# Optimization experiments

Hardware: AMD Instinct MI355X
Metric: run time of the kernel (lower is better)

The kernel has to match this reference:

```python
import jax, jax.numpy as jnp
import numpy as np
from jax import lax

B, C, T, S = 32, 122, 500, 13
WID, EMB, PROJ = 80, 8, 1024
HID = 768  # (H=1)*(W=96)*(E=8) after CNN
EPS = 1e-5
DN = ('NCHW', 'OIHW', 'NCHW')


def setup_inputs() -> dict:
    key = jax.random.key(0)
    ks = jax.random.split(key, 24)
    f32 = jnp.float32
    def n(k, shape, scale):
        return (jax.random.normal(k, shape, dtype=f32) * scale).astype(f32)
    return {
        'x': jax.random.normal(ks[0], (B, C, T), dtype=f32),
        'subject_ids': jax.random.randint(ks[1], (B,), 0, S, dtype=jnp.int32),
        'W_sub': n(ks[2], (S, T, T), 0.04),      # nn.Linear(500,500) weight per subject
        'b_sub': n(ks[3], (S, T), 0.02),
        'conv1_w': n(ks[4], (WID, 1, 1, 5), 0.3),
        'conv1_b': n(ks[5], (WID,), 0.02),
        'bn1_g': 1.0 + n(ks[6], (WID,), 0.1),
        'bn1_b': n(ks[7], (WID,), 0.1),
        'bn1_m': n(ks[8], (WID,), 0.1),
        'bn1_v': 0.5 + jax.random.uniform(ks[9], (WID,), dtype=f32),
        'conv2_w': n(ks[10], (WID, WID, C, 1), 0.01),
        'conv2_b': n(ks[11], (WID,), 0.02),
        'bn2_g': 1.0 + n(ks[12], (WID,), 0.1),
        'bn2_b': n(ks[13], (WID,), 0.1),
        'bn2_m': n(ks[14], (WID,), 0.1),
        'bn2_v': 0.5 + jax.random.uniform(ks[15], (WID,), dtype=f32),
        'proj_w': n(ks[16], (EMB, WID, 1, 1), 0.1),
        'proj_b': n(ks[17], (EMB,), 0.02),
        'mlp1_w': n(ks[18], (PROJ, HID), 0.03),
        'mlp1_b': n(ks[19], (PROJ,), 0.02),
        'mlp2_w': n(ks[20], (PROJ, PROJ), 0.03),
        'mlp2_b': n(ks[21], (PROJ,), 0.02),
        'ln_g': 1.0 + n(ks[22], (PROJ,), 0.05),
        'ln_b': n(ks[23], (PROJ,), 0.05),
    }


def _bn(h, g, b, m, v):
    # eval-mode BatchNorm2d over channel axis 1
    scale = (g / jnp.sqrt(v + EPS))[None, :, None, None]
    shift = (b - m * g / jnp.sqrt(v + EPS))[None, :, None, None]
    return h * scale + shift


def _forward(x, subject_ids, W_sub, b_sub, conv1_w, conv1_b, bn1_g, bn1_b, bn1_m, bn1_v,
             conv2_w, conv2_b, bn2_g, bn2_b, bn2_m, bn2_v, proj_w, proj_b,
             mlp1_w, mlp1_b, mlp2_w, mlp2_b, ln_g, ln_b):
    # --- per-subject routing: gather each sample's Linear(500,500) and apply ---
    Wg = W_sub[subject_ids]                       # [B,T,T] (out,in)
    bg = b_sub[subject_ids]                       # [B,T]
    out = jnp.einsum('bcs,bts->bct', x, Wg) + bg[:, None, :]
    # --- spatio-temporal CNN (eval mode: dropout = identity) ---
    h = out[:, None, :, :]                        # [B,1,C,T]
    h = lax.conv_general_dilated(h, conv1_w, (1, 1), 'VALID', dimension_numbers=DN)
    h = h + conv1_b[None, :, None, None]          # [B,80,122,496]
    h = lax.reduce_window(h, 0.0, lax.add, (1, 1, 1, 17), (1, 1, 1, 5), 'VALID') / 17.0  # [B,80,122,96]
    h = jax.nn.elu(_bn(h, bn1_g, bn1_b, bn1_m, bn1_v))
    h = lax.conv_general_dilated(h, conv2_w, (1, 1), 'VALID', dimension_numbers=DN)
    h = h + conv2_b[None, :, None, None]          # [B,80,1,96]
    h = jax.nn.elu(_bn(h, bn2_g, bn2_b, bn2_m, bn2_v))
    h = lax.conv_general_dilated(h, proj_w, (1, 1), 'VALID', dimension_numbers=DN)
    h = h + proj_b[None, :, None, None]           # [B,8,1,96]
    z = jnp.transpose(h, (0, 2, 3, 1)).reshape(h.shape[0], -1)  # [B,768]
    # --- MLP projector: Linear -> Residual(GELU+Linear) -> LayerNorm ---
    z1 = z @ mlp1_w.T + mlp1_b                    # [B,1024]
    r = jax.nn.gelu(z1, approximate=False) @ mlp2_w.T + mlp2_b
    y = z1 + r
    mu = jnp.mean(y, axis=-1, keepdims=True)
    var = jnp.var(y, axis=-1, keepdims=True)
    return (y - mu) / jnp.sqrt(var + EPS) * ln_g + ln_b


def reference(x, subject_ids, W_sub, b_sub, conv1_w, conv1_b, bn1_g, bn1_b, bn1_m, bn1_v,
              conv2_w, conv2_b, bn2_g, bn2_b, bn2_m, bn2_v, proj_w, proj_b,
              mlp1_w, mlp1_b, mlp2_w, mlp2_b, ln_g, ln_b):
    return _forward(x, subject_ids, W_sub, b_sub, conv1_w, conv1_b, bn1_g, bn1_b, bn1_m, bn1_v,
                    conv2_w, conv2_b, bn2_g, bn2_b, bn2_m, bn2_v, proj_w, proj_b,
                    mlp1_w, mlp1_b, mlp2_w, mlp2_b, ln_g, ln_b)
```

## Files before the change

### kernel.cpp

```cpp
#include <hip/hip_runtime.h>
#include <math.h>

#define BB 32
#define CC 122
#define TT 500
#define SS 13
#define WID 80
#define EMB 8
#define PROJ 1024
#define HID 768
#define TP 96
#define EPSF 1e-5f
#define KP 9760
#define KBN 305
#define KSPLIT 16

typedef float f32x4 __attribute__((ext_vector_type(4)));
typedef __bf16 bf16x8 __attribute__((ext_vector_type(8)));
typedef unsigned short u16x8 __attribute__((ext_vector_type(8)));
union BF8 { u16x8 u; bf16x8 b; };

__device__ __forceinline__ unsigned short f2bf(float f) {
    union { float f; unsigned u; } v; v.f = f;
    unsigned r = v.u + 0x7FFFu + ((v.u >> 16) & 1u);
    return (unsigned short)(r >> 16);
}

__device__ __forceinline__ float eluf(float x) {
    return x > 0.f ? x : __expf(x) - 1.f;
}

#define OFF_E    ((size_t)0)
#define OFF_XB   ((size_t)1952000)
#define OFF_WB   ((size_t)3000576)
#define OFF_W2P  ((size_t)4704512)
#define OFF_P    ((size_t)5094912)
#define OFF_PART ((size_t)20086272)
#define OFF_Z    ((size_t)24018432)
#define OFF_Z1   ((size_t)24030720)
#define OFF_G    ((size_t)24063488)
#define OFF_Y    ((size_t)24079872)
#define OFF_W1B  ((size_t)24112640)
#define OFF_W2B  ((size_t)24505856)
#define OFF_WCB  ((size_t)25030144)
#define OFF_B1F  ((size_t)25031424)
#define OFF_SC2  ((size_t)25031504)
#define OFF_SH2  ((size_t)25031584)

#define NPK_X  (2097152)
#define NPK_W  (3407872)
#define NPK_W2 (780800)
#define NPK_M1 (786432)
#define NPK_M2 (1048576)
#define NPK_TOT (NPK_X + NPK_W + NPK_W2 + NPK_M1 + NPK_M2)

__global__ __launch_bounds__(256) void k_pack(const float* __restrict__ x,
                                              const float* __restrict__ W_sub,
                                              const float* __restrict__ conv2_w,
                                              const float* __restrict__ mlp1_w,
                                              const float* __restrict__ mlp2_w,
                                              const float* __restrict__ conv1_w, const float* __restrict__ conv1_b,
                                              const float* __restrict__ g1, const float* __restrict__ b1,
                                              const float* __restrict__ m1, const float* __restrict__ v1,
                                              const float* __restrict__ conv2_b, const float* __restrict__ g2,
                                              const float* __restrict__ b2, const float* __restrict__ m2,
                                              const float* __restrict__ v2,
                                              unsigned short* __restrict__ xb,
                                              unsigned short* __restrict__ wb,
                                              unsigned short* __restrict__ w2p,
                                              unsigned short* __restrict__ w1b,
                                              unsigned short* __restrict__ w2b,
                                              unsigned short* __restrict__ wcb, float* __restrict__ bias1f,
                                              float* __restrict__ scale2, float* __restrict__ shift2f) {
    if (blockIdx.x == 0) {
        int o = threadIdx.x;
        if (o < WID) {
            float s1 = g1[o] * rsqrtf(v1[o] + EPSF);
            float sh1 = b1[o] - m1[o] * s1;
            #pragma unroll
            for (int d = 0; d < 21; d++) {
                int klo = d - 16; if (klo < 0) klo = 0;
                int khi = d;      if (khi > 4) khi = 4;
                float acc = 0.f;
                for (int k = klo; k <= khi; k++) acc += conv1_w[o*5 + k];
                wcb[o*32 + d] = f2bf(acc * s1 * (1.f/17.f));
            }
            #pragma unroll
            for (int d = 21; d < 32; d++) wcb[o*32 + d] = 0;
            bias1f[o] = conv1_b[o] * s1 + sh1;
            float s2 = g2[o] * rsqrtf(v2[o] + EPSF);
            scale2[o] = s2;
            shift2f[o] = conv2_b[o] * s2 + (b2[o] - m2[o] * s2);
        }
    }
    size_t idx = (size_t)blockIdx.x * 256 + threadIdx.x;
    if (idx >= (size_t)NPK_TOT) return;
    if (idx < NPK_X) {
        int s = idx & 511, c = (idx >> 9) & 127, b = idx >> 16;
        float v = (c < CC && s < TT) ? x[((size_t)b * CC + c) * TT + s] : 0.f;
        xb[idx] = f2bf(v);
    } else if (idx < NPK_X + NPK_W) {
        size_t j = idx - NPK_X;
        int s = j & 511, t = (j >> 9) & 511, sub = j >> 18;
        float v = (t < TT && s < TT) ? W_sub[((size_t)sub * TT + t) * TT + s] : 0.f;
        wb[j] = f2bf(v);
    } else if (idx < NPK_X + NPK_W + NPK_W2) {
        size_t j = idx - NPK_X - NPK_W;
        int o = (int)(j / KP);
        int k = (int)(j % KP);
        int c = k / WID, op = k % WID;
        w2p[j] = f2bf(conv2_w[((size_t)(o * WID + op)) * CC + c]);
    } else if (idx < NPK_X + NPK_W + NPK_W2 + NPK_M1) {
        size_t j = idx - NPK_X - NPK_W - NPK_W2;
        w1b[j] = f2bf(mlp1_w[j]);
    } else {
        size_t j = idx - NPK_X - NPK_W - NPK_W2 - NPK_M1;
        w2b[j] = f2bf(mlp2_w[j]);
    }
}

__global__ __launch_bounds__(256) void k_einsum(const unsigned short* __restrict__ xb,
                                                const unsigned short* __restrict__ wb,
                                                const int* __restrict__ sid,
                                                const float* __restrict__ b_sub,
                                                float* __restrict__ oute) {
    int t0 = blockIdx.x * 64, b = blockIdx.y;
    int s = sid[b];
    int tid = threadIdx.x, w = tid >> 6, lr = tid & 15, lg = (tid >> 4) & 3;
    const unsigned short* A0 = xb + ((size_t)(b * 128 + w * 32 + lr)) * 512 + 8 * lg;
    const unsigned short* Bb = wb + (size_t)s * 262144 + 8 * lg;
    f32x4 acc[2][4] = {};
    for (int kb = 0; kb < 512; kb += 32) {
        BF8 a0, a1;
        a0.u = *(const u16x8*)(A0 + kb);
        a1.u = *(const u16x8*)(A0 + 16 * 512 + kb);
        #pragma unroll
        for (int nt = 0; nt < 4; nt++) {
            BF8 bf; bf.u = *(const u16x8*)(Bb + (size_t)(t0 + nt * 16 + lr) * 512 + kb);
            acc[0][nt] = __builtin_amdgcn_mfma_f32_16x16x32_bf16(a0.b, bf.b, acc[0][nt], 0, 0, 0);
            acc[1][nt] = __builtin_amdgcn_mfma_f32_16x16x32_bf16(a1.b, bf.b, acc[1][nt], 0, 0, 0);
        }
    }
    const float* bg = b_sub + (size_t)s * TT;
    #pragma unroll
    for (int nt = 0; nt < 4; nt++) {
        int t = t0 + nt * 16 + lr;
        if (t < TT) {
            float bias = bg[t];
            #pragma unroll
            for (int mt = 0; mt < 2; mt++) {
                int crow = w * 32 + mt * 16 + 4 * lg;
                #pragma unroll
                for (int r = 0; r < 4; r++) {
                    int c = crow + r;
                    if (c < CC) oute[((size_t)b * CC + c) * TT + t] = acc[mt][nt][r] + bias;
                }
            }
        }
    }
}

__global__ __launch_bounds__(256) void k_fir2(const float* __restrict__ oute,
                                              const unsigned short* __restrict__ wcb,
                                              const float* __restrict__ b1f,
                                              unsigned short* __restrict__ p) {
    __shared__ float e2[2][512];
    int cp = blockIdx.x, b = blockIdx.y;
    int tid = threadIdx.x;
    int w = tid >> 6, lr = tid & 15, lg = (tid >> 4) & 3;
    if (tid < 250) {
        int cc = tid / 125, i = tid % 125;
        ((float4*)e2[cc])[i] = ((const float4*)(oute + ((size_t)b * CC + cp * 2 + cc) * TT))[i];
    }
    if (tid >= 232) {
        int j = tid - 232; int cc = j / 12, i = 500 + (j % 12);
        e2[cc][i] = 0.f;
    }
    BF8 af[5]; float4 bf4[5];
    #pragma unroll
    for (int ot = 0; ot < 5; ot++) {
        af[ot].u = *(const u16x8*)(wcb + (ot * 16 + lr) * 32 + 8 * lg);
        bf4[ot] = *(const float4*)(b1f + ot * 16 + 4 * lg);
    }
    __syncthreads();
    #pragma unroll
    for (int ui = 0; ui < 3; ui++) {
        int u = w + 4 * ui;
        int cc = u / 6, tt = u % 6;
        int t = tt * 16 + lr;
        const float* ew = e2[cc] + 5 * t + 8 * lg;
        BF8 bfr;
        #pragma unroll
        for (int j = 0; j < 8; j++) bfr.u[j] = f2bf(ew[j]);
        f32x4 acc[5] = {};
        #pragma unroll
        for (int ot = 0; ot < 5; ot++)
            acc[ot] = __builtin_amdgcn_mfma_f32_16x16x32_bf16(af[ot].b, bfr.b, acc[ot], 0, 0, 0);
        int c = cp * 2 + cc;
        unsigned short* pr = p + ((size_t)b * TP + t) * KP + (size_t)c * WID + 4 * lg;
        #pragma unroll
        for (int ot = 0; ot < 5; ot++) {
            union { unsigned short s[4]; uint2 v; } pk;
            #pragma unroll
            for (int r = 0; r < 4; r++) pk.s[r] = f2bf(eluf(acc[ot][r] + bf4[ot][r]));
            *(uint2*)(pr + ot * 16) = pk.v;
        }
    }
}

__global__ __launch_bounds__(384) void k_conv2(const unsigned short* __restrict__ p,
                                               const unsigned short* __restrict__ w2p,
                                               float* __restrict__ part) {
    int chunk = blockIdx.x, b = blockIdx.y;
    int tid = threadIdx.x, w = tid >> 6, l = tid & 63, lr = l & 15, lg = l >> 4;
    int kb0 = (chunk * KBN) / KSPLIT;
    int kb1 = ((chunk + 1) * KBN) / KSPLIT;
    const unsigned short* Brow = p + ((size_t)(b * TP + w * 16 + lr)) * KP + 8 * lg;
    const unsigned short* Arow = w2p + (size_t)lr * KP + 8 * lg;
    f32x4 acc[5] = {};
    for (int kb = kb0; kb < kb1; kb++) {
        int ko = kb * 32;
        BF8 bf; bf.u = *(const u16x8*)(Brow + ko);
        #pragma unroll
        for (int mt = 0; mt < 5; mt++) {
            BF8 af; af.u = *(const u16x8*)(Arow + (size_t)mt * 16 * KP + ko);
            acc[mt] = __builtin_amdgcn_mfma_f32_16x16x32_bf16(af.b, bf.b, acc[mt], 0, 0, 0);
        }
    }
    float* pp = part + ((size_t)(chunk * BB + b) * WID) * TP;
    int t = w * 16 + lr;
    #pragma unroll
    for (int mt = 0; mt < 5; mt++) {
        int ob = mt * 16 + 4 * lg;
        #pragma unroll
        for (int r = 0; r < 4; r++)
            pp[(size_t)(ob + r) * TP + t] = acc[mt][r];
    }
}

__global__ __launch_bounds__(256) void k_redproj(const float* __restrict__ part,
                                                 const float* __restrict__ scale2,
                                                 const float* __restrict__ shift2f,
                                                 const float* __restrict__ pw,
                                                 const float* __restrict__ pb,
                                                 unsigned short* __restrict__ zbf) {
    __shared__ float ly[WID * TP];
    __shared__ float lw[EMB * WID];
    int b = blockIdx.x, tid = threadIdx.x;
    for (int i = tid; i < EMB * WID; i += 256) lw[i] = pw[i];
    for (int i = tid; i < WID * TP; i += 256) {
        float acc = 0.f;
        #pragma unroll
        for (int ks = 0; ks < KSPLIT; ks++)
            acc += part[(size_t)(ks * BB + b) * (WID * TP) + i];
        int o = i / TP;
        ly[i] = eluf(acc * scale2[o] + shift2f[o]);
    }
    __syncthreads();
    #pragma unroll
    for (int rep = 0; rep < 3; rep++) {
        int j = tid + 256 * rep;
        int e = j & 7, t = j >> 3;
        float acc = pb[e];
        #pragma unroll 10
        for (int o = 0; o < WID; o++) acc = fmaf(ly[o * TP + t], lw[e * WID + o], acc);
        zbf[(size_t)b * HID + j] = f2bf(acc);
    }
}

__global__ __launch_bounds__(256) void k_mlp1(const unsigned short* __restrict__ zbf,
                                              const unsigned short* __restrict__ w1b,
                                              const float* __restrict__ bias,
                                              float* __restrict__ z1,
                                              unsigned short* __restrict__ gbf) {
    __shared__ float accb[2][64][4];
    int tid = threadIdx.x, w = tid >> 6, l = tid & 63, lr = l & 15, lg = l >> 4;
    int mt = w & 1, kh = w >> 1;
    int pcol = blockIdx.x * 16 + lr;
    const unsigned short* wr = w1b + (size_t)pcol * HID + kh * 384 + 8 * lg;
    const unsigned short* za = zbf + (size_t)(mt * 16 + lr) * HID + kh * 384 + 8 * lg;
    f32x4 acc = {};
    for (int kb = 0; kb < 384; kb += 32) {
        BF8 bf; bf.u = *(const u16x8*)(wr + kb);
        BF8 a;  a.u  = *(const u16x8*)(za + kb);
        acc = __builtin_amdgcn_mfma_f32_16x16x32_bf16(a.b, bf.b, acc, 0, 0, 0);
    }
    if (kh == 1) {
        #pragma unroll
        for (int r = 0; r < 4; r++) accb[mt][l][r] = acc[r];
    }
    __syncthreads();
    if (kh == 0) {
        float bs = bias[pcol];
        #pragma unroll
        for (int r = 0; r < 4; r++) {
            int row = mt * 16 + 4 * lg + r;
            float v = acc[r] + accb[mt][l][r] + bs;
            z1[(size_t)row * PROJ + pcol] = v;
            gbf[(size_t)row * PROJ + pcol] = f2bf(0.5f * v * (1.f + erff(v * 0.70710678118654752f)));
        }
    }
}

__global__ __launch_bounds__(256) void k_mlp2(const unsigned short* __restrict__ gbf,
                                              const float* __restrict__ z1,
                                              const unsigned short* __restrict__ w2b,
                                              const float* __restrict__ bias,
                                              float* __restrict__ y) {
    __shared__ float accb[2][64][4];
    int tid = threadIdx.x, w = tid >> 6, l = tid & 63, lr = l & 15, lg = l >> 4;
    int mt = w & 1, kh = w >> 1;
    int q = blockIdx.x * 16 + lr;
    const unsigned short* wr = w2b + (size_t)q * PROJ + kh * 512 + 8 * lg;
    const unsigned short* ga = gbf + (size_t)(mt * 16 + lr) * PROJ + kh * 512 + 8 * lg;
    f32x4 acc = {};
    for (int kb = 0; kb < 512; kb += 32) {
        BF8 bf; bf.u = *(const u16x8*)(wr + kb);
        BF8 a;  a.u  = *(const u16x8*)(ga + kb);
        acc = __builtin_amdgcn_mfma_f32_16x16x32_bf16(a.b, bf.b, acc, 0, 0, 0);
    }
    if (kh == 1) {
        #pragma unroll
        for (int r = 0; r < 4; r++) accb[mt][l][r] = acc[r];
    }
    __syncthreads();
    if (kh == 0) {
        float bs = bias[q];
        #pragma unroll
        for (int r = 0; r < 4; r++) {
            int row = mt * 16 + 4 * lg + r;
            y[(size_t)row * PROJ + q] = acc[r] + accb[mt][l][r] + bs + z1[(size_t)row * PROJ + q];
        }
    }
}

__global__ __launch_bounds__(256) void k_ln(const float* __restrict__ y,
                                            const float* __restrict__ lg,
                                            const float* __restrict__ lb,
                                            float* __restrict__ out) {
    int b = blockIdx.x, tid = threadIdx.x;
    const float4* yr = (const float4*)(y + (size_t)b * PROJ);
    float4 v = yr[tid];
    float s  = v.x + v.y + v.z + v.w;
    float sq = v.x*v.x + v.y*v.y + v.z*v.z + v.w*v.w;
    #pragma unroll
    for (int off = 32; off > 0; off >>= 1) {
        s  += __shfl_down(s, off);
        sq += __shfl_down(sq, off);
    }
    __shared__ float ss[4], ssq[4];
    int wv = tid >> 6, lane = tid & 63;
    if (lane == 0) { ss[wv] = s; ssq[wv] = sq; }
    __syncthreads();
    __shared__ float smu, sinv;
    if (tid == 0) {
        float Sm = ss[0] + ss[1] + ss[2] + ss[3];
        float Sq = ssq[0] + ssq[1] + ssq[2] + ssq[3];
        float mu = Sm * (1.f / PROJ);
        float var = Sq * (1.f / PROJ) - mu * mu;
        smu = mu;
        sinv = rsqrtf(var + EPSF);
    }
    __syncthreads();
    float mu = smu, inv = sinv;
    float4 g4 = ((const float4*)lg)[tid];
    float4 b4 = ((const float4*)lb)[tid];
    float4 o4;
    o4.x = (v.x - mu) * inv * g4.x + b4.x;
    o4.y = (v.y - mu) * inv * g4.y + b4.y;
    o4.z = (v.z - mu) * inv * g4.z + b4.z;
    o4.w = (v.w - mu) * inv * g4.w + b4.w;
    ((float4*)(out + (size_t)b * PROJ))[tid] = o4;
}

extern "C" void kernel_launch(void* const* d_in, const int* in_sizes, int n_in,
                              void* d_out, int out_size, void* d_ws, size_t ws_size,
                              hipStream_t stream) {
    const float* x        = (const float*)d_in[0];
    const int*   sid      = (const int*)  d_in[1];
    const float* W_sub    = (const float*)d_in[2];
    const float* b_sub    = (const float*)d_in[3];
    const float* conv1_w  = (const float*)d_in[4];
    const float* conv1_b  = (const float*)d_in[5];
    const float* bn1_g    = (const float*)d_in[6];
    const float* bn1_b    = (const float*)d_in[7];
    const float* bn1_m    = (const float*)d_in[8];
    const float* bn1_v    = (const float*)d_in[9];
    const float* conv2_w  = (const float*)d_in[10];
    const float* conv2_b  = (const float*)d_in[11];
    const float* bn2_g    = (const float*)d_in[12];
    const float* bn2_b    = (const float*)d_in[13];
    const float* bn2_m    = (const float*)d_in[14];
    const float* bn2_v    = (const float*)d_in[15];
    const float* proj_w   = (const float*)d_in[16];
    const float* proj_b   = (const float*)d_in[17];
    const float* mlp1_w   = (const float*)d_in[18];
    const float* mlp1_b   = (const float*)d_in[19];
    const float* mlp2_w   = (const float*)d_in[20];
    const float* mlp2_b   = (const float*)d_in[21];
    const float* ln_g     = (const float*)d_in[22];
    const float* ln_b     = (const float*)d_in[23];
    float* out = (float*)d_out;
    float* ws  = (float*)d_ws;

    float* ws_e    = ws + OFF_E;
    unsigned short* ws_xb  = (unsigned short*)(ws + OFF_XB);
    unsigned short* ws_wb  = (unsigned short*)(ws + OFF_WB);
    unsigned short* ws_w2p = (unsigned short*)(ws + OFF_W2P);
    unsigned short* ws_p   = (unsigned short*)(ws + OFF_P);
    float* ws_part = ws + OFF_PART;
    unsigned short* ws_zbf = (unsigned short*)(ws + OFF_Z);
    float* ws_z1   = ws + OFF_Z1;
    unsigned short* ws_gbf = (unsigned short*)(ws + OFF_G);
    float* ws_y    = ws + OFF_Y;
    unsigned short* ws_w1b = (unsigned short*)(ws + OFF_W1B);
    unsigned short* ws_w2b = (unsigned short*)(ws + OFF_W2B);
    unsigned short* ws_wcb = (unsigned short*)(ws + OFF_WCB);
    float* ws_b1f  = ws + OFF_B1F;
    float* ws_sc2  = ws + OFF_SC2;
    float* ws_sh2  = ws + OFF_SH2;

    hipLaunchKernelGGL(k_pack, dim3((NPK_TOT + 255) / 256), dim3(256), 0, stream,
                       x, W_sub, conv2_w, mlp1_w, mlp2_w,
                       conv1_w, conv1_b, bn1_g, bn1_b, bn1_m, bn1_v,
                       conv2_b, bn2_g, bn2_b, bn2_m, bn2_v,
                       ws_xb, ws_wb, ws_w2p, ws_w1b, ws_w2b,
                       ws_wcb, ws_b1f, ws_sc2, ws_sh2);

    hipLaunchKernelGGL(k_einsum, dim3(8, BB), dim3(256), 0, stream,
                       ws_xb, ws_wb, sid, b_sub, ws_e);

    hipLaunchKernelGGL(k_fir2, dim3(CC / 2, BB), dim3(256), 0, stream,
                       ws_e, ws_wcb, ws_b1f, ws_p);

    hipLaunchKernelGGL(k_conv2, dim3(KSPLIT, BB), dim3(384), 0, stream,
                       ws_p, ws_w2p, ws_part);

    hipLaunchKernelGGL(k_redproj, dim3(BB), dim3(256), 0, stream,
                       ws_part, ws_sc2, ws_sh2, proj_w, proj_b, ws_zbf);

    hipLaunchKernelGGL(k_mlp1, dim3(PROJ / 16), dim3(256), 0, stream,
                       ws_zbf, ws_w1b, mlp1_b, ws_z1, ws_gbf);

    hipLaunchKernelGGL(k_mlp2, dim3(PROJ / 16), dim3(256), 0, stream,
                       ws_gbf, ws_z1, ws_w2b, mlp2_b, ws_y);

    hipLaunchKernelGGL(k_ln, dim3(BB), dim3(256), 0, stream,
                       ws_y, ln_g, ln_b, out);
}
```

Baseline: 231.9 us.

## Store conv2 B operand in MFMA fragment order via LDS-staged transpose

k_fir2 now stages its ELU/bf16 output tile in shared memory and writes it to global in a pre-swizzled layout that matches the per-lane MFMA B fragment order. k_conv2 then reads each k-block with a single contiguous 16-byte load per lane, instead of loads strided by KP. The aim is fully coalesced reads in the conv2 GEMM and contiguous writes in fir2. The cost is extra LDS use, one more barrier, and a transposing copy loop in fir2.

```diff
diff --git a/kernel.cpp b/kernel.cpp
--- a/kernel.cpp
+++ b/kernel.cpp
@@ -163,8 +163,9 @@
 __global__ __launch_bounds__(256) void k_fir2(const float* __restrict__ oute,
                                               const unsigned short* __restrict__ wcb,
                                               const float* __restrict__ b1f,
-                                              unsigned short* __restrict__ p) {
+                                              unsigned short* __restrict__ p2) {
     __shared__ float e2[2][512];
+    __shared__ unsigned short pt[96][164];
     int cp = blockIdx.x, b = blockIdx.y;
     int tid = threadIdx.x;
     int w = tid >> 6, lr = tid & 15, lg = (tid >> 4) & 3;
@@ -196,31 +197,41 @@
         #pragma unroll
         for (int ot = 0; ot < 5; ot++)
             acc[ot] = __builtin_amdgcn_mfma_f32_16x16x32_bf16(af[ot].b, bfr.b, acc[ot], 0, 0, 0);
-        int c = cp * 2 + cc;
-        unsigned short* pr = p + ((size_t)b * TP + t) * KP + (size_t)c * WID + 4 * lg;
         #pragma unroll
         for (int ot = 0; ot < 5; ot++) {
             union { unsigned short s[4]; uint2 v; } pk;
             #pragma unroll
             for (int r = 0; r < 4; r++) pk.s[r] = f2bf(eluf(acc[ot][r] + bf4[ot][r]));
-            *(uint2*)(pr + ot * 16) = pk.v;
-        }
-    }
-}
-
-__global__ __launch_bounds__(384) void k_conv2(const unsigned short* __restrict__ p,
+            *(uint2*)&pt[t][cc * 80 + ot * 16 + 4 * lg] = pk.v;
+        }
+    }
+    __syncthreads();
+    const size_t base = ((size_t)b * KBN + 5 * (size_t)cp) * 3072;
+    int q = 2 * tid;
+    int l = q >> 3, jj = q & 7;
+    int prow_lo = l & 15;
+    int pcol_off = ((l >> 4) << 3) + jj;
+    #pragma unroll
+    for (int r = 0; r < 30; r++) {
+        int kbl = r / 6, tt2 = r % 6;
+        unsigned v = *(const unsigned*)&pt[tt2 * 16 + prow_lo][kbl * 32 + pcol_off];
+        *(unsigned*)(p2 + base + (size_t)(kbl * 6 + tt2) * 512 + q) = v;
+    }
+}
+
+__global__ __launch_bounds__(384) void k_conv2(const unsigned short* __restrict__ p2,
                                                const unsigned short* __restrict__ w2p,
                                                float* __restrict__ part) {
     int chunk = blockIdx.x, b = blockIdx.y;
     int tid = threadIdx.x, w = tid >> 6, l = tid & 63, lr = l & 15, lg = l >> 4;
     int kb0 = (chunk * KBN) / KSPLIT;
     int kb1 = ((chunk + 1) * KBN) / KSPLIT;
-    const unsigned short* Brow = p + ((size_t)(b * TP + w * 16 + lr)) * KP + 8 * lg;
+    const unsigned short* Bp = p2 + (size_t)b * KBN * 3072 + (size_t)w * 512 + (size_t)l * 8;
     const unsigned short* Arow = w2p + (size_t)lr * KP + 8 * lg;
     f32x4 acc[5] = {};
     for (int kb = kb0; kb < kb1; kb++) {
+        BF8 bf; bf.u = *(const u16x8*)(Bp + (size_t)kb * 3072);
         int ko = kb * 32;
-        BF8 bf; bf.u = *(const u16x8*)(Brow + ko);
         #pragma unroll
         for (int mt = 0; mt < 5; mt++) {
             BF8 af; af.u = *(const u16x8*)(Arow + (size_t)mt * 16 * KP + ko);
@@ -407,7 +418,7 @@
     unsigned short* ws_xb  = (unsigned short*)(ws + OFF_XB);
     unsigned short* ws_wb  = (unsigned short*)(ws + OFF_WB);
     unsigned short* ws_w2p = (unsigned short*)(ws + OFF_W2P);
-    unsigned short* ws_p   = (unsigned short*)(ws + OFF_P);
+    unsigned short* ws_p2  = (unsigned short*)(ws + OFF_P);
     float* ws_part = ws + OFF_PART;
     unsigned short* ws_zbf = (unsigned short*)(ws + OFF_Z);
     float* ws_z1   = ws + OFF_Z1;
@@ -431,10 +442,10 @@
                        ws_xb, ws_wb, sid, b_sub, ws_e);
 
     hipLaunchKernelGGL(k_fir2, dim3(CC / 2, BB), dim3(256), 0, stream,
-                       ws_e, ws_wcb, ws_b1f, ws_p);
+                       ws_e, ws_wcb, ws_b1f, ws_p2);
 
     hipLaunchKernelGGL(k_conv2, dim3(KSPLIT, BB), dim3(384), 0, stream,
-                       ws_p, ws_w2p, ws_part);
+                       ws_p2, ws_w2p, ws_part);
 
     hipLaunchKernelGGL(k_redproj, dim3(BB), dim3(256), 0, stream,
                        ws_part, ws_sc2, ws_sh2, proj_w, proj_b, ws_zbf);
```

Result: faster. 221.8 us (-4.3%).
